# Optimization experiments

Measured on AMD Instinct MI355X. Metric: run time of the kernel, lower is better.

## Reference

```python
import jax, jax.numpy as jnp
import numpy as np
import math

B, N, DIM = 2, 4096, 256
NUM_HEADS = 8
HEAD_DIM = DIM // NUM_HEADS
WINDOW = 7  # default window_size in create_local_mask


def local_mask(seq_len: int, window_size: int = WINDOW) -> jnp.ndarray:
    """Boolean [N,N] mask: True where attention is allowed (2D grid locality)."""
    grid = int(math.isqrt(seq_len))
    idx = jnp.arange(seq_len)
    row, col = idx // grid, idx % grid
    half = window_size // 2
    ok_row = jnp.abs(row[:, None] - row[None, :]) <= half
    ok_col = jnp.abs(col[:, None] - col[None, :]) <= half
    return ok_row & ok_col


def setup_inputs() -> dict:
    key = jax.random.key(0)
    k1, k2, k3, k4 = jax.random.split(key, 4)
    x = jax.random.normal(k1, (B, N, DIM), dtype=jnp.float32)
    W_qkv = jax.random.normal(k2, (3 * DIM, DIM), dtype=jnp.float32) * (DIM ** -0.5)
    W_proj = jax.random.normal(k3, (DIM, DIM), dtype=jnp.float32) * (DIM ** -0.5)
    b_proj = jax.random.normal(k4, (DIM,), dtype=jnp.float32) * 0.01
    temperature = jnp.ones((1,), dtype=jnp.float32)
    return {"x": x, "W_qkv": W_qkv, "W_proj": W_proj, "b_proj": b_proj,
            "temperature": temperature}


def reference(x, W_qkv, W_proj, b_proj, temperature):
    Bb, Nn, C = x.shape
    scale = HEAD_DIM ** -0.5
    # qkv linear (no bias): [B,N,3C] -> [3,B,H,N,hd]
    qkv = (x @ W_qkv.T).reshape(Bb, Nn, 3, NUM_HEADS, HEAD_DIM)
    qkv = jnp.transpose(qkv, (2, 0, 3, 1, 4))
    q, k, v = qkv[0], qkv[1], qkv[2]
    # scores with learnable temperature
    attn = jnp.einsum('bhqd,bhkd->bhqk', q, k) * (scale * temperature[0])
    mask = local_mask(Nn)  # training path: N > 100 -> mask applied
    attn = jnp.where(mask[None, None, :, :], attn, -jnp.inf)
    attn = jax.nn.softmax(attn, axis=-1)
    out = jnp.einsum('bhqk,bhkd->bhqd', attn, v)  # [B,H,N,hd]
    out = jnp.transpose(out, (0, 2, 1, 3)).reshape(Bb, Nn, C)
    return out @ W_proj.T + b_proj
```

## Files before the change

kernel.cpp:

```cpp
#include <hip/hip_runtime.h>
#include <hip/hip_bf16.h>
#include <hip/hip_fp16.h>
#include <math.h>

#define DIM   256
#define NHEAD 8
#define HD    32
#define NTOK  4096
#define GRD   64
#define BATCH 2
#define MTOT  (BATCH * NTOK)

typedef __attribute__((ext_vector_type(8))) short bf16x8;
typedef __attribute__((ext_vector_type(4))) float f32x4;
typedef _Float16 h8 __attribute__((ext_vector_type(8)));
typedef _Float16 h2v __attribute__((ext_vector_type(2)));

#if defined(__has_builtin)
#if __has_builtin(__builtin_amdgcn_fdot2)
#define HAVE_DOT2 1
#endif
#endif
#ifndef HAVE_DOT2
#define HAVE_DOT2 0
#endif

static __device__ __forceinline__ unsigned short f2b(float f) {
  __hip_bfloat16 h = __float2bfloat16(f);
  union { __hip_bfloat16 h; unsigned short u; } cv;
  cv.h = h;
  return cv.u;
}

static __device__ __forceinline__ bf16x8 pack8(float4 a0, float4 a1) {
  union { bf16x8 v; unsigned short u[8]; } o;
  o.u[0] = f2b(a0.x); o.u[1] = f2b(a0.y); o.u[2] = f2b(a0.z); o.u[3] = f2b(a0.w);
  o.u[4] = f2b(a1.x); o.u[5] = f2b(a1.y); o.u[6] = f2b(a1.z); o.u[7] = f2b(a1.w);
  return o.v;
}

__global__ __launch_bounds__(256) void gemm_qkv(const float* __restrict__ A,
                                                const float* __restrict__ Bw,
                                                _Float16* __restrict__ Cout) {
  const int K = 256, N = 768;
  __shared__ __hip_bfloat16 As[128 * 40];
  __shared__ __hip_bfloat16 Bs[128 * 40];
  const int tid = threadIdx.x;
  const int l = tid & 63, w = tid >> 6;
  const int bm = blockIdx.y * 128, bn = blockIdx.x * 128;
  const int wr = w >> 1, wc = w & 1;
  const int lr = l & 15, kh = l >> 4;
  const int lrow = l >> 2, lcol = (l & 3) * 8;

  f32x4 acc[4][4];
  #pragma unroll
  for (int i = 0; i < 4; ++i)
    #pragma unroll
    for (int j = 0; j < 4; ++j)
      acc[i][j] = (f32x4){0.f, 0.f, 0.f, 0.f};

  for (int k0 = 0; k0 < K; k0 += 32) {
    #pragma unroll
    for (int i = 0; i < 2; ++i) {
      const int r0 = (w * 2 + i) * 16;
      const float* ga = A  + (size_t)(bm + r0 + lrow) * K + k0 + lcol;
      const float* gb = Bw + (size_t)(bn + r0 + lrow) * K + k0 + lcol;
      float4 a0 = *(const float4*)ga, a1 = *(const float4*)(ga + 4);
      float4 b0 = *(const float4*)gb, b1 = *(const float4*)(gb + 4);
      *(bf16x8*)&As[(r0 + lrow) * 40 + lcol] = pack8(a0, a1);
      *(bf16x8*)&Bs[(r0 + lrow) * 40 + lcol] = pack8(b0, b1);
    }
    __syncthreads();

    bf16x8 af[4], bfr[4];
    #pragma unroll
    for (int f = 0; f < 4; ++f) {
      af[f]  = *(const bf16x8*)&As[(wr * 64 + f * 16 + lr) * 40 + kh * 8];
      bfr[f] = *(const bf16x8*)&Bs[(wc * 64 + f * 16 + lr) * 40 + kh * 8];
    }
    #pragma unroll
    for (int fi = 0; fi < 4; ++fi)
      #pragma unroll
      for (int fj = 0; fj < 4; ++fj)
        acc[fi][fj] = __builtin_amdgcn_mfma_f32_16x16x32_bf16(af[fi], bfr[fj], acc[fi][fj], 0, 0, 0);
    __syncthreads();
  }

  #pragma unroll
  for (int fi = 0; fi < 4; ++fi)
    #pragma unroll
    for (int fj = 0; fj < 4; ++fj)
      #pragma unroll
      for (int rr = 0; rr < 4; ++rr) {
        const int m = bm + wr * 64 + fi * 16 + kh * 4 + rr;
        const int n = bn + wc * 64 + fj * 16 + lr;
        const int sel = n >> 8, rem = n & 255;
        const int hh = rem >> 5, d = rem & 31;
        const int bb = m >> 12, tok = m & 4095;
        Cout[((size_t)(sel * 16 + bb * 8 + hh) * NTOK + tok) * HD + d] =
            (_Float16)acc[fi][fj][rr];
      }
}

__global__ __launch_bounds__(256) void gemm_proj(const __hip_bfloat16* __restrict__ A,
                                                 const float* __restrict__ Bw,
                                                 const float* __restrict__ bias,
                                                 float* __restrict__ Cout) {
  const int K = 256, N = 256;
  __shared__ __hip_bfloat16 As[128 * 32];
  __shared__ __hip_bfloat16 Bs[128 * 40];
  const int tid = threadIdx.x;
  const int l = tid & 63, w = tid >> 6;
  const int bm = blockIdx.y * 128, bn = blockIdx.x * 128;
  const int wr = w >> 1, wc = w & 1;
  const int lr = l & 15, kh = l >> 4;
  const int lrow = l >> 2, lcol = (l & 3) * 8;

  f32x4 acc[4][4];
  #pragma unroll
  for (int i = 0; i < 4; ++i)
    #pragma unroll
    for (int j = 0; j < 4; ++j)
      acc[i][j] = (f32x4){0.f, 0.f, 0.f, 0.f};

  for (int k0 = 0; k0 < K; k0 += 32) {
    #pragma unroll
    for (int i = 0; i < 2; ++i) {
      const int r0 = (w * 2 + i) * 16;
      const __hip_bfloat16* ga = A + (size_t)(bm + r0 + lrow) * K + k0 + lcol;
      __builtin_amdgcn_global_load_lds(
          (const __attribute__((address_space(1))) void*)ga,
          (__attribute__((address_space(3))) void*)&As[r0 * 32], 16, 0, 0);
      const float* gb = Bw + (size_t)(bn + r0 + lrow) * K + k0 + lcol;
      float4 b0 = *(const float4*)gb, b1 = *(const float4*)(gb + 4);
      *(bf16x8*)&Bs[(r0 + lrow) * 40 + lcol] = pack8(b0, b1);
    }
    __syncthreads();

    bf16x8 af[4], bfr[4];
    #pragma unroll
    for (int f = 0; f < 4; ++f) {
      af[f]  = *(const bf16x8*)&As[(wr * 64 + f * 16 + lr) * 32 + kh * 8];
      bfr[f] = *(const bf16x8*)&Bs[(wc * 64 + f * 16 + lr) * 40 + kh * 8];
    }
    #pragma unroll
    for (int fi = 0; fi < 4; ++fi)
      #pragma unroll
      for (int fj = 0; fj < 4; ++fj)
        acc[fi][fj] = __builtin_amdgcn_mfma_f32_16x16x32_bf16(af[fi], bfr[fj], acc[fi][fj], 0, 0, 0);
    __syncthreads();
  }

  #pragma unroll
  for (int fi = 0; fi < 4; ++fi)
    #pragma unroll
    for (int fj = 0; fj < 4; ++fj)
      #pragma unroll
      for (int rr = 0; rr < 4; ++rr) {
        const int m = bm + wr * 64 + fi * 16 + kh * 4 + rr;
        const int n = bn + wc * 64 + fj * 16 + lr;
        Cout[(size_t)m * N + n] = acc[fi][fj][rr] + bias[n];
      }
}

__global__ __launch_bounds__(512) void local_attn(const _Float16* __restrict__ qkv,
                                                  const float* __restrict__ temp,
                                                  __hip_bfloat16* __restrict__ attn_out) {
  __shared__ _Float16 Ks[512 * 32];
  __shared__ _Float16 Vs[512 * 32];

  const int P = blockIdx.x;
  const int L = (P & 7) * 64 + (P >> 3);
  const int plane = L >> 5, rp = L & 31;
  const int b = plane >> 3, h = plane & 7;
  const int t = threadIdx.x;
  const int qr = t >> 8, c = (t >> 2) & 63, s = t & 3;
  const int r = rp * 2 + qr;

  const float scale = 0.17677669529663687f * temp[0];

  const _Float16* qplane = qkv + (size_t)(b * 8 + h) * (NTOK * HD);
  const _Float16* kplane = qkv + (size_t)(16 + b * 8 + h) * (NTOK * HD);
  const _Float16* vplane = qkv + (size_t)(32 + b * 8 + h) * (NTOK * HD);

  {
    const int rbase = rp * 2 - 3;
    const int wbase = t & ~63;
    #pragma unroll
    for (int i = 0; i < 4; ++i) {
      const int id = i * 512 + t;
      const int drp = id >> 8;
      const int tokloc = (id >> 2) & 63;
      const int jjp = id & 3;
      const int x = ((tokloc >> 1) ^ drp) & 3;
      const int jj = jjp ^ x;
      int row = rbase + drp;
      row = row < 0 ? 0 : (row > 63 ? 63 : row);
      const _Float16* src = kplane + (size_t)row * 2048 + tokloc * 32 + jj * 8;
      const _Float16* srv = vplane + (size_t)row * 2048 + tokloc * 32 + jj * 8;
      const int dbase = (i * 512 + wbase) * 8;
      __builtin_amdgcn_global_load_lds(
          (const __attribute__((address_space(1))) void*)src,
          (__attribute__((address_space(3))) void*)&Ks[dbase], 16, 0, 0);
      __builtin_amdgcn_global_load_lds(
          (const __attribute__((address_space(1))) void*)srv,
          (__attribute__((address_space(3))) void*)&Vs[dbase], 16, 0, 0);
    }
  }

  union { h8 v; h2v p[4]; } qu[4];
  {
    const _Float16* qrp_ = qplane + (size_t)(r * GRD + c) * HD;
    #pragma unroll
    for (int jj = 0; jj < 4; ++jj) qu[jj].v = *(const h8*)&qrp_[jj * 8];
  }
  __syncthreads();

  const char* KB = (const char*)Ks;
  const char* VB = (const char*)Vs;
  float sc[14];
  int bs[14];
  float mx = -INFINITY;
  const int ndr = (s < 3) ? 2 : 1;
  #pragma unroll
  for (int i = 0; i < 2; ++i) {
    const int dr = s - 3 + 4 * i;
    const int drp = dr + 3 + qr;
    const int rr = r + dr;
    const bool rowok = (i < ndr) && (rr >= 0) && (rr < GRD);
    #pragma unroll
    for (int dc = -3; dc <= 3; ++dc) {
      const int cc = c + dc;
      const bool ok = rowok && (cc >= 0) && (cc < GRD);
      int tk = drp * 64 + cc;
      tk = tk < 0 ? 0 : (tk > 511 ? 511 : tk);
      const int x = ((tk >> 1) ^ (tk >> 6)) & 3;
      const int sb = (tk << 6) ^ (x << 4);
      bs[i * 7 + dc + 3] = sb;
      float dot = 0.f;
      #pragma unroll
      for (int jj = 0; jj < 4; ++jj) {
        union { h8 v; h2v p[4]; } kk;
        kk.v = *(const h8*)(KB + (sb ^ (jj << 4)));
        #pragma unroll
        for (int kx = 0; kx < 4; ++kx) {
#if HAVE_DOT2
          dot = __builtin_amdgcn_fdot2(kk.p[kx], qu[jj].p[kx], dot, false);
#else
          dot = fmaf((float)kk.p[kx][0], (float)qu[jj].p[kx][0], dot);
          dot = fmaf((float)kk.p[kx][1], (float)qu[jj].p[kx][1], dot);
#endif
        }
      }
      const float v = ok ? dot * scale : -INFINITY;
      sc[i * 7 + dc + 3] = v;
      mx = fmaxf(mx, v);
    }
  }

  mx = fmaxf(mx, __shfl_xor(mx, 1));
  mx = fmaxf(mx, __shfl_xor(mx, 2));

  float psum = 0.f;
  #pragma unroll
  for (int i = 0; i < 14; ++i) {
    float e = __expf(sc[i] - mx);
    sc[i] = e;
    psum += e;
  }
  psum += __shfl_xor(psum, 1);
  psum += __shfl_xor(psum, 2);
  const float inv = 1.0f / psum;

  float o[HD];
  #pragma unroll
  for (int i = 0; i < HD; ++i) o[i] = 0.f;

  #pragma unroll
  for (int e = 0; e < 14; ++e) {
    const float p = sc[e];
    const int sb = bs[e];
    #pragma unroll
    for (int jj = 0; jj < 4; ++jj) {
      union { h8 v; h2v p2[4]; } vv;
      vv.v = *(const h8*)(VB + (sb ^ (jj << 4)));
      #pragma unroll
      for (int kx = 0; kx < 4; ++kx) {
        o[jj * 8 + kx * 2 + 0] = fmaf(p, (float)vv.p2[kx][0], o[jj * 8 + kx * 2 + 0]);
        o[jj * 8 + kx * 2 + 1] = fmaf(p, (float)vv.p2[kx][1], o[jj * 8 + kx * 2 + 1]);
      }
    }
  }

  #pragma unroll
  for (int d = 0; d < HD; ++d) {
    o[d] += __shfl_xor(o[d], 1);
    o[d] += __shfl_xor(o[d], 2);
  }

  union { uint4 u; unsigned short sh[8]; } pk;
  #pragma unroll
  for (int j = 0; j < 8; ++j) pk.sh[j] = f2b(o[s * 8 + j] * inv);
  __hip_bfloat16* dst = attn_out + ((size_t)(b * NTOK + r * GRD + c)) * DIM + h * HD + s * 8;
  *(uint4*)dst = pk.u;
}

extern "C" void kernel_launch(void* const* d_in, const int* in_sizes, int n_in,
                              void* d_out, int out_size, void* d_ws, size_t ws_size,
                              hipStream_t stream) {
  const float* x     = (const float*)d_in[0];
  const float* Wqkv  = (const float*)d_in[1];
  const float* Wproj = (const float*)d_in[2];
  const float* bproj = (const float*)d_in[3];
  const float* temp  = (const float*)d_in[4];
  float* out = (float*)d_out;

  char* ws = (char*)d_ws;
  _Float16* qkv_f16       = (_Float16*)ws;
  __hip_bfloat16* attn_bf = (__hip_bfloat16*)(ws + 25165824);

  {
    dim3 grid(3 * DIM / 128, MTOT / 128);
    gemm_qkv<<<grid, 256, 0, stream>>>(x, Wqkv, qkv_f16);
  }
  local_attn<<<BATCH * NHEAD * (GRD / 2), 512, 0, stream>>>(qkv_f16, temp, attn_bf);

  {
    dim3 grid(DIM / 128, MTOT / 128);
    gemm_proj<<<grid, 256, 0, stream>>>(attn_bf, Wproj, bproj, out);
  }
}
```

Measured before the change: 49.79 us.

## Shrink GEMM M-tiles to 64 and redistribute attention PV work across lanes

```diff
diff --git a/kernel.cpp b/kernel.cpp
--- a/kernel.cpp
+++ b/kernel.cpp
@@ -15,6 +15,7 @@
 typedef __attribute__((ext_vector_type(4))) float f32x4;
 typedef _Float16 h8 __attribute__((ext_vector_type(8)));
 typedef _Float16 h2v __attribute__((ext_vector_type(2)));
+typedef __fp16 fp16x2 __attribute__((ext_vector_type(2)));
 
 #if defined(__has_builtin)
 #if __has_builtin(__builtin_amdgcn_fdot2)
@@ -42,44 +43,47 @@
 __global__ __launch_bounds__(256) void gemm_qkv(const float* __restrict__ A,
                                                 const float* __restrict__ Bw,
                                                 _Float16* __restrict__ Cout) {
-  const int K = 256, N = 768;
-  __shared__ __hip_bfloat16 As[128 * 40];
+  const int K = 256;
+  __shared__ __hip_bfloat16 As[64 * 40];
   __shared__ __hip_bfloat16 Bs[128 * 40];
   const int tid = threadIdx.x;
   const int l = tid & 63, w = tid >> 6;
-  const int bm = blockIdx.y * 128, bn = blockIdx.x * 128;
+  const int bm = blockIdx.y * 64, bn = blockIdx.x * 128;
   const int wr = w >> 1, wc = w & 1;
   const int lr = l & 15, kh = l >> 4;
-  const int lrow = l >> 2, lcol = (l & 3) * 8;
-
-  f32x4 acc[4][4];
-  #pragma unroll
-  for (int i = 0; i < 4; ++i)
+  const int lrow = tid >> 2, lcol = (tid & 3) * 8;
+
+  f32x4 acc[2][4];
+  #pragma unroll
+  for (int i = 0; i < 2; ++i)
     #pragma unroll
     for (int j = 0; j < 4; ++j)
       acc[i][j] = (f32x4){0.f, 0.f, 0.f, 0.f};
 
   for (int k0 = 0; k0 < K; k0 += 32) {
+    {
+      const float* ga = A + (size_t)(bm + lrow) * K + k0 + lcol;
+      float4 a0 = *(const float4*)ga, a1 = *(const float4*)(ga + 4);
+      *(bf16x8*)&As[lrow * 40 + lcol] = pack8(a0, a1);
+    }
     #pragma unroll
     for (int i = 0; i < 2; ++i) {
-      const int r0 = (w * 2 + i) * 16;
-      const float* ga = A  + (size_t)(bm + r0 + lrow) * K + k0 + lcol;
-      const float* gb = Bw + (size_t)(bn + r0 + lrow) * K + k0 + lcol;
-      float4 a0 = *(const float4*)ga, a1 = *(const float4*)(ga + 4);
+      const int row = i * 64 + lrow;
+      const float* gb = Bw + (size_t)(bn + row) * K + k0 + lcol;
       float4 b0 = *(const float4*)gb, b1 = *(const float4*)(gb + 4);
-      *(bf16x8*)&As[(r0 + lrow) * 40 + lcol] = pack8(a0, a1);
-      *(bf16x8*)&Bs[(r0 + lrow) * 40 + lcol] = pack8(b0, b1);
+      *(bf16x8*)&Bs[row * 40 + lcol] = pack8(b0, b1);
     }
     __syncthreads();
 
-    bf16x8 af[4], bfr[4];
-    #pragma unroll
-    for (int f = 0; f < 4; ++f) {
-      af[f]  = *(const bf16x8*)&As[(wr * 64 + f * 16 + lr) * 40 + kh * 8];
+    bf16x8 af[2], bfr[4];
+    #pragma unroll
+    for (int f = 0; f < 2; ++f)
+      af[f] = *(const bf16x8*)&As[(wr * 32 + f * 16 + lr) * 40 + kh * 8];
+    #pragma unroll
+    for (int f = 0; f < 4; ++f)
       bfr[f] = *(const bf16x8*)&Bs[(wc * 64 + f * 16 + lr) * 40 + kh * 8];
-    }
-    #pragma unroll
-    for (int fi = 0; fi < 4; ++fi)
+    #pragma unroll
+    for (int fi = 0; fi < 2; ++fi)
       #pragma unroll
       for (int fj = 0; fj < 4; ++fj)
         acc[fi][fj] = __builtin_amdgcn_mfma_f32_16x16x32_bf16(af[fi], bfr[fj], acc[fi][fj], 0, 0, 0);
@@ -87,12 +91,12 @@
   }
 
   #pragma unroll
-  for (int fi = 0; fi < 4; ++fi)
+  for (int fi = 0; fi < 2; ++fi)
     #pragma unroll
     for (int fj = 0; fj < 4; ++fj)
       #pragma unroll
       for (int rr = 0; rr < 4; ++rr) {
-        const int m = bm + wr * 64 + fi * 16 + kh * 4 + rr;
+        const int m = bm + wr * 32 + fi * 16 + kh * 4 + rr;
         const int n = bn + wc * 64 + fj * 16 + lr;
         const int sel = n >> 8, rem = n & 255;
         const int hh = rem >> 5, d = rem & 31;
@@ -107,44 +111,47 @@
                                                  const float* __restrict__ bias,
                                                  float* __restrict__ Cout) {
   const int K = 256, N = 256;
-  __shared__ __hip_bfloat16 As[128 * 32];
+  __shared__ __hip_bfloat16 As[64 * 32];
   __shared__ __hip_bfloat16 Bs[128 * 40];
   const int tid = threadIdx.x;
   const int l = tid & 63, w = tid >> 6;
-  const int bm = blockIdx.y * 128, bn = blockIdx.x * 128;
+  const int bm = blockIdx.y * 64, bn = blockIdx.x * 128;
   const int wr = w >> 1, wc = w & 1;
   const int lr = l & 15, kh = l >> 4;
-  const int lrow = l >> 2, lcol = (l & 3) * 8;
-
-  f32x4 acc[4][4];
-  #pragma unroll
-  for (int i = 0; i < 4; ++i)
+  const int lrow = tid >> 2, lcol = (tid & 3) * 8;
+
+  f32x4 acc[2][4];
+  #pragma unroll
+  for (int i = 0; i < 2; ++i)
     #pragma unroll
     for (int j = 0; j < 4; ++j)
       acc[i][j] = (f32x4){0.f, 0.f, 0.f, 0.f};
 
   for (int k0 = 0; k0 < K; k0 += 32) {
-    #pragma unroll
-    for (int i = 0; i < 2; ++i) {
-      const int r0 = (w * 2 + i) * 16;
-      const __hip_bfloat16* ga = A + (size_t)(bm + r0 + lrow) * K + k0 + lcol;
+    {
+      const __hip_bfloat16* ga = A + (size_t)(bm + lrow) * K + k0 + lcol;
       __builtin_amdgcn_global_load_lds(
           (const __attribute__((address_space(1))) void*)ga,
-          (__attribute__((address_space(3))) void*)&As[r0 * 32], 16, 0, 0);
-      const float* gb = Bw + (size_t)(bn + r0 + lrow) * K + k0 + lcol;
+          (__attribute__((address_space(3))) void*)&As[w * 512], 16, 0, 0);
+    }
+    #pragma unroll
+    for (int i = 0; i < 2; ++i) {
+      const int row = i * 64 + lrow;
+      const float* gb = Bw + (size_t)(bn + row) * K + k0 + lcol;
       float4 b0 = *(const float4*)gb, b1 = *(const float4*)(gb + 4);
-      *(bf16x8*)&Bs[(r0 + lrow) * 40 + lcol] = pack8(b0, b1);
+      *(bf16x8*)&Bs[row * 40 + lcol] = pack8(b0, b1);
     }
     __syncthreads();
 
-    bf16x8 af[4], bfr[4];
-    #pragma unroll
-    for (int f = 0; f < 4; ++f) {
-      af[f]  = *(const bf16x8*)&As[(wr * 64 + f * 16 + lr) * 32 + kh * 8];
+    bf16x8 af[2], bfr[4];
+    #pragma unroll
+    for (int f = 0; f < 2; ++f)
+      af[f] = *(const bf16x8*)&As[(wr * 32 + f * 16 + lr) * 32 + kh * 8];
+    #pragma unroll
+    for (int f = 0; f < 4; ++f)
       bfr[f] = *(const bf16x8*)&Bs[(wc * 64 + f * 16 + lr) * 40 + kh * 8];
-    }
-    #pragma unroll
-    for (int fi = 0; fi < 4; ++fi)
+    #pragma unroll
+    for (int fi = 0; fi < 2; ++fi)
       #pragma unroll
       for (int fj = 0; fj < 4; ++fj)
         acc[fi][fj] = __builtin_amdgcn_mfma_f32_16x16x32_bf16(af[fi], bfr[fj], acc[fi][fj], 0, 0, 0);
@@ -152,12 +159,12 @@
   }
 
   #pragma unroll
-  for (int fi = 0; fi < 4; ++fi)
+  for (int fi = 0; fi < 2; ++fi)
     #pragma unroll
     for (int fj = 0; fj < 4; ++fj)
       #pragma unroll
       for (int rr = 0; rr < 4; ++rr) {
-        const int m = bm + wr * 64 + fi * 16 + kh * 4 + rr;
+        const int m = bm + wr * 32 + fi * 16 + kh * 4 + rr;
         const int n = bn + wc * 64 + fj * 16 + lr;
         Cout[(size_t)m * N + n] = acc[fi][fj][rr] + bias[n];
       }
@@ -219,7 +226,6 @@
   const char* KB = (const char*)Ks;
   const char* VB = (const char*)Vs;
   float sc[14];
-  int bs[14];
   float mx = -INFINITY;
   const int ndr = (s < 3) ? 2 : 1;
   #pragma unroll
@@ -236,7 +242,6 @@
       tk = tk < 0 ? 0 : (tk > 511 ? 511 : tk);
       const int x = ((tk >> 1) ^ (tk >> 6)) & 3;
       const int sb = (tk << 6) ^ (x << 4);
-      bs[i * 7 + dc + 3] = sb;
       float dot = 0.f;
       #pragma unroll
       for (int jj = 0; jj < 4; ++jj) {
@@ -272,35 +277,55 @@
   psum += __shfl_xor(psum, 2);
   const float inv = 1.0f / psum;
 
-  float o[HD];
-  #pragma unroll
-  for (int i = 0; i < HD; ++i) o[i] = 0.f;
-
-  #pragma unroll
-  for (int e = 0; e < 14; ++e) {
-    const float p = sc[e];
-    const int sb = bs[e];
-    #pragma unroll
-    for (int jj = 0; jj < 4; ++jj) {
-      union { h8 v; h2v p2[4]; } vv;
-      vv.v = *(const h8*)(VB + (sb ^ (jj << 4)));
-      #pragma unroll
-      for (int kx = 0; kx < 4; ++kx) {
-        o[jj * 8 + kx * 2 + 0] = fmaf(p, (float)vv.p2[kx][0], o[jj * 8 + kx * 2 + 0]);
-        o[jj * 8 + kx * 2 + 1] = fmaf(p, (float)vv.p2[kx][1], o[jj * 8 + kx * 2 + 1]);
+  unsigned int mine[7], r1v[7], r2a[7], r2b[7];
+  #pragma unroll
+  for (int j = 0; j < 7; ++j) {
+    fp16x2 hp = __builtin_amdgcn_cvt_pkrtz(sc[2 * j] * inv, sc[2 * j + 1] * inv);
+    union { fp16x2 h; unsigned int u; } cv; cv.h = hp;
+    mine[j] = cv.u;
+  }
+  #pragma unroll
+  for (int j = 0; j < 7; ++j) r1v[j] = (unsigned)__shfl_xor((int)mine[j], 1);
+  #pragma unroll
+  for (int j = 0; j < 7; ++j) r2a[j] = (unsigned)__shfl_xor((int)mine[j], 2);
+  #pragma unroll
+  for (int j = 0; j < 7; ++j) r2b[j] = (unsigned)__shfl_xor((int)r1v[j], 2);
+
+  float o[8];
+  #pragma unroll
+  for (int i = 0; i < 8; ++i) o[i] = 0.f;
+
+  #pragma unroll
+  for (int ss = 0; ss < 4; ++ss) {
+    const unsigned int* set = (ss == 0) ? mine : (ss == 1) ? r1v
+                             : (ss == 2) ? r2a : r2b;
+    const int sp = s ^ ss;
+    #pragma unroll
+    for (int j = 0; j < 7; ++j) {
+      union { unsigned int u; h2v h; } pp; pp.u = set[j];
+      #pragma unroll
+      for (int half = 0; half < 2; ++half) {
+        const int slot = 2 * j + half;
+        const int ii = slot / 7;
+        const int dc = (slot % 7) - 3;
+        const float p = (float)pp.h[half];
+        int tk = (sp + 4 * ii + qr) * 64 + c + dc;
+        tk = tk < 0 ? 0 : (tk > 511 ? 511 : tk);
+        const int x = ((tk >> 1) ^ (tk >> 6)) & 3;
+        union { h8 v; h2v p2[4]; } vv;
+        vv.v = *(const h8*)(VB + (tk << 6) + (((s ^ x) & 3) << 4));
+        #pragma unroll
+        for (int kx = 0; kx < 4; ++kx) {
+          o[kx * 2 + 0] = fmaf(p, (float)vv.p2[kx][0], o[kx * 2 + 0]);
+          o[kx * 2 + 1] = fmaf(p, (float)vv.p2[kx][1], o[kx * 2 + 1]);
+        }
       }
     }
   }
 
-  #pragma unroll
-  for (int d = 0; d < HD; ++d) {
-    o[d] += __shfl_xor(o[d], 1);
-    o[d] += __shfl_xor(o[d], 2);
-  }
-
   union { uint4 u; unsigned short sh[8]; } pk;
   #pragma unroll
-  for (int j = 0; j < 8; ++j) pk.sh[j] = f2b(o[s * 8 + j] * inv);
+  for (int j = 0; j < 8; ++j) pk.sh[j] = f2b(o[j]);
   __hip_bfloat16* dst = attn_out + ((size_t)(b * NTOK + r * GRD + c)) * DIM + h * HD + s * 8;
   *(uint4*)dst = pk.u;
 }
@@ -320,13 +345,13 @@
   __hip_bfloat16* attn_bf = (__hip_bfloat16*)(ws + 25165824);
 
   {
-    dim3 grid(3 * DIM / 128, MTOT / 128);
+    dim3 grid(3 * DIM / 128, MTOT / 64);
     gemm_qkv<<<grid, 256, 0, stream>>>(x, Wqkv, qkv_f16);
   }
   local_attn<<<BATCH * NHEAD * (GRD / 2), 512, 0, stream>>>(qkv_f16, temp, attn_bf);
 
   {
-    dim3 grid(DIM / 128, MTOT / 128);
+    dim3 grid(DIM / 128, MTOT / 64);
     gemm_proj<<<grid, 256, 0, stream>>>(attn_bf, Wproj, bproj, out);
   }
 }
```

Measured after the change: 110.1 us. +121.2%, slower.

## Rewrite local attention with bf16 MFMA and online softmax, transposed V layout

Applied to the files above, without the earlier changes.

```diff
diff --git a/kernel.cpp b/kernel.cpp
--- a/kernel.cpp
+++ b/kernel.cpp
@@ -1,6 +1,5 @@
 #include <hip/hip_runtime.h>
 #include <hip/hip_bf16.h>
-#include <hip/hip_fp16.h>
 #include <math.h>
 
 #define DIM   256
@@ -10,20 +9,10 @@
 #define GRD   64
 #define BATCH 2
 #define MTOT  (BATCH * NTOK)
+#define PLANE (NTOK * HD)
 
 typedef __attribute__((ext_vector_type(8))) short bf16x8;
 typedef __attribute__((ext_vector_type(4))) float f32x4;
-typedef _Float16 h8 __attribute__((ext_vector_type(8)));
-typedef _Float16 h2v __attribute__((ext_vector_type(2)));
-
-#if defined(__has_builtin)
-#if __has_builtin(__builtin_amdgcn_fdot2)
-#define HAVE_DOT2 1
-#endif
-#endif
-#ifndef HAVE_DOT2
-#define HAVE_DOT2 0
-#endif
 
 static __device__ __forceinline__ unsigned short f2b(float f) {
   __hip_bfloat16 h = __float2bfloat16(f);
@@ -32,6 +21,12 @@
   return cv.u;
 }
 
+static __device__ __forceinline__ unsigned cvtpk_bf16(float lo, float hi) {
+  unsigned r;
+  asm("v_cvt_pk_bf16_f32 %0, %1, %2" : "=v"(r) : "v"(lo), "v"(hi));
+  return r;
+}
+
 static __device__ __forceinline__ bf16x8 pack8(float4 a0, float4 a1) {
   union { bf16x8 v; unsigned short u[8]; } o;
   o.u[0] = f2b(a0.x); o.u[1] = f2b(a0.y); o.u[2] = f2b(a0.z); o.u[3] = f2b(a0.w);
@@ -39,12 +34,17 @@
   return o.v;
 }
 
+#define GLDS16(SRC, DST) __builtin_amdgcn_global_load_lds( \
+    (const __attribute__((address_space(1))) void*)(SRC),  \
+    (__attribute__((address_space(3))) void*)(DST), 16, 0, 0)
+
 __global__ __launch_bounds__(256) void gemm_qkv(const float* __restrict__ A,
                                                 const float* __restrict__ Bw,
-                                                _Float16* __restrict__ Cout) {
-  const int K = 256, N = 768;
-  __shared__ __hip_bfloat16 As[128 * 40];
-  __shared__ __hip_bfloat16 Bs[128 * 40];
+                                                unsigned short* __restrict__ Cout) {
+  const int K = 256;
+  __shared__ __align__(16) char smem[34816];
+  __hip_bfloat16* As = (__hip_bfloat16*)smem;
+  __hip_bfloat16* Bs = (__hip_bfloat16*)(smem + 10240);
   const int tid = threadIdx.x;
   const int l = tid & 63, w = tid >> 6;
   const int bm = blockIdx.y * 128, bn = blockIdx.x * 128;
@@ -86,20 +86,48 @@
     __syncthreads();
   }
 
-  #pragma unroll
-  for (int fi = 0; fi < 4; ++fi)
-    #pragma unroll
-    for (int fj = 0; fj < 4; ++fj)
-      #pragma unroll
-      for (int rr = 0; rr < 4; ++rr) {
-        const int m = bm + wr * 64 + fi * 16 + kh * 4 + rr;
-        const int n = bn + wc * 64 + fj * 16 + lr;
-        const int sel = n >> 8, rem = n & 255;
-        const int hh = rem >> 5, d = rem & 31;
-        const int bb = m >> 12, tok = m & 4095;
-        Cout[((size_t)(sel * 16 + bb * 8 + hh) * NTOK + tok) * HD + d] =
-            (_Float16)acc[fi][fj][rr];
-      }
+  if (blockIdx.x < 4) {
+    #pragma unroll
+    for (int fi = 0; fi < 4; ++fi)
+      #pragma unroll
+      for (int fj = 0; fj < 4; ++fj)
+        #pragma unroll
+        for (int rr = 0; rr < 4; ++rr) {
+          const int m = bm + wr * 64 + fi * 16 + kh * 4 + rr;
+          const int n = bn + wc * 64 + fj * 16 + lr;
+          const int sel = n >> 8, rem = n & 255;
+          const int hh = rem >> 5, d = rem & 31;
+          const int bb = m >> 12, tok = m & 4095;
+          Cout[(size_t)(sel * 16 + bb * 8 + hh) * PLANE + tok * 32 + d] =
+              f2b(acc[fi][fj][rr]);
+        }
+  } else {
+    unsigned short* Ts = (unsigned short*)smem;
+    #pragma unroll
+    for (int fi = 0; fi < 4; ++fi)
+      #pragma unroll
+      for (int fj = 0; fj < 4; ++fj)
+        #pragma unroll
+        for (int rr = 0; rr < 4; ++rr) {
+          const int tokl = wr * 64 + fi * 16 + kh * 4 + rr;
+          const int dl   = wc * 64 + fj * 16 + lr;
+          Ts[tokl * 136 + dl] = f2b(acc[fi][fj][rr]);
+        }
+    __syncthreads();
+    const int dl = tid >> 1, th = (tid & 1) * 64;
+    const int dg = (bn - 512) + dl;
+    const int hh = dg >> 5, dd = dg & 31;
+    const int bb = bm >> 12, tokb = bm & 4095;
+    unsigned short* vt = Cout + (size_t)(32 + bb * 8 + hh) * PLANE + dd * 4096 + tokb + th;
+    #pragma unroll
+    for (int j = 0; j < 8; ++j) {
+      union { bf16x8 v; unsigned short u[8]; } o;
+      #pragma unroll
+      for (int e = 0; e < 8; ++e)
+        o.u[e] = Ts[(th + j * 8 + e) * 136 + dl];
+      *(bf16x8*)(vt + j * 8) = o.v;
+    }
+  }
 }
 
 __global__ __launch_bounds__(256) void gemm_proj(const __hip_bfloat16* __restrict__ A,
@@ -128,9 +156,7 @@
     for (int i = 0; i < 2; ++i) {
       const int r0 = (w * 2 + i) * 16;
       const __hip_bfloat16* ga = A + (size_t)(bm + r0 + lrow) * K + k0 + lcol;
-      __builtin_amdgcn_global_load_lds(
-          (const __attribute__((address_space(1))) void*)ga,
-          (__attribute__((address_space(3))) void*)&As[r0 * 32], 16, 0, 0);
+      GLDS16(ga, &As[r0 * 32]);
       const float* gb = Bw + (size_t)(bn + r0 + lrow) * K + k0 + lcol;
       float4 b0 = *(const float4*)gb, b1 = *(const float4*)(gb + 4);
       *(bf16x8*)&Bs[(r0 + lrow) * 40 + lcol] = pack8(b0, b1);
@@ -163,146 +189,145 @@
       }
 }
 
-__global__ __launch_bounds__(512) void local_attn(const _Float16* __restrict__ qkv,
-                                                  const float* __restrict__ temp,
-                                                  __hip_bfloat16* __restrict__ attn_out) {
-  __shared__ _Float16 Ks[512 * 32];
-  __shared__ _Float16 Vs[512 * 32];
+__global__ __launch_bounds__(256) void local_attn_mfma(
+    const unsigned short* __restrict__ qkv, const float* __restrict__ temp,
+    unsigned short* __restrict__ attn_out) {
+  __shared__ __align__(16) unsigned short Ks[448 * 32];
+  __shared__ __align__(16) unsigned short Vt[32 * 512];
 
   const int P = blockIdx.x;
-  const int L = (P & 7) * 64 + (P >> 3);
-  const int plane = L >> 5, rp = L & 31;
-  const int b = plane >> 3, h = plane & 7;
-  const int t = threadIdx.x;
-  const int qr = t >> 8, c = (t >> 2) & 63, s = t & 3;
-  const int r = rp * 2 + qr;
+  const int L = (P & 7) * 128 + (P >> 3);
+  const int b = L >> 9, h = (L >> 6) & 7, r = L & 63;
+  const int tid = threadIdx.x;
+  const int l = tid & 63, wv = tid >> 6;
+  const int q15 = l & 15, sg = l >> 4;
 
   const float scale = 0.17677669529663687f * temp[0];
 
-  const _Float16* qplane = qkv + (size_t)(b * 8 + h) * (NTOK * HD);
-  const _Float16* kplane = qkv + (size_t)(16 + b * 8 + h) * (NTOK * HD);
-  const _Float16* vplane = qkv + (size_t)(32 + b * 8 + h) * (NTOK * HD);
-
-  {
-    const int rbase = rp * 2 - 3;
-    const int wbase = t & ~63;
-    #pragma unroll
-    for (int i = 0; i < 4; ++i) {
-      const int id = i * 512 + t;
-      const int drp = id >> 8;
-      const int tokloc = (id >> 2) & 63;
-      const int jjp = id & 3;
-      const int x = ((tokloc >> 1) ^ drp) & 3;
-      const int jj = jjp ^ x;
-      int row = rbase + drp;
-      row = row < 0 ? 0 : (row > 63 ? 63 : row);
-      const _Float16* src = kplane + (size_t)row * 2048 + tokloc * 32 + jj * 8;
-      const _Float16* srv = vplane + (size_t)row * 2048 + tokloc * 32 + jj * 8;
-      const int dbase = (i * 512 + wbase) * 8;
-      __builtin_amdgcn_global_load_lds(
-          (const __attribute__((address_space(1))) void*)src,
-          (__attribute__((address_space(3))) void*)&Ks[dbase], 16, 0, 0);
-      __builtin_amdgcn_global_load_lds(
-          (const __attribute__((address_space(1))) void*)srv,
-          (__attribute__((address_space(3))) void*)&Vs[dbase], 16, 0, 0);
-    }
-  }
-
-  union { h8 v; h2v p[4]; } qu[4];
-  {
-    const _Float16* qrp_ = qplane + (size_t)(r * GRD + c) * HD;
-    #pragma unroll
-    for (int jj = 0; jj < 4; ++jj) qu[jj].v = *(const h8*)&qrp_[jj * 8];
-  }
+  const unsigned short* qplane  = qkv + (size_t)(b * 8 + h) * PLANE;
+  const unsigned short* kplane  = qplane + (size_t)16 * PLANE;
+  const unsigned short* vtplane = qplane + (size_t)32 * PLANE;
+
+  #pragma unroll
+  for (int i = 0; i < 7; ++i) {
+    const int ch = i * 256 + tid;
+    const int tok = ch >> 2, jjp = ch & 3;
+    const int ri = tok >> 6, kloc = tok & 63;
+    int rr = r - 3 + ri; rr = rr < 0 ? 0 : (rr > 63 ? 63 : rr);
+    const int jl = jjp ^ ((tok >> 1) & 3);
+    const unsigned short* src = kplane + (size_t)(rr * 64 + kloc) * 32 + jl * 8;
+    GLDS16(src, &Ks[(i * 256 + (tid & ~63)) * 8]);
+  }
+  #pragma unroll
+  for (int i = 0; i < 8; ++i) {
+    const int ch = i * 256 + tid;
+    const int d = ch >> 6, chp = ch & 63;
+    const int chl = chp ^ (d & 7);
+    const int ri = chl >> 3, part = chl & 7;
+    int rr = r - 3 + ri; rr = rr < 0 ? 0 : (rr > 63 ? 63 : rr);
+    const unsigned short* src = vtplane + (size_t)d * 4096 + rr * 64 + part * 8;
+    GLDS16(src, &Vt[(i * 256 + (tid & ~63)) * 8]);
+  }
+
+  const bf16x8 qf = *(const bf16x8*)(qplane + (size_t)(r * 64 + wv * 16 + q15) * 32 + sg * 8);
+
   __syncthreads();
 
-  const char* KB = (const char*)Ks;
-  const char* VB = (const char*)Vs;
-  float sc[14];
-  int bs[14];
-  float mx = -INFINITY;
-  const int ndr = (s < 3) ? 2 : 1;
-  #pragma unroll
-  for (int i = 0; i < 2; ++i) {
-    const int dr = s - 3 + 4 * i;
-    const int drp = dr + 3 + qr;
-    const int rr = r + dr;
-    const bool rowok = (i < ndr) && (rr >= 0) && (rr < GRD);
-    #pragma unroll
-    for (int dc = -3; dc <= 3; ++dc) {
-      const int cc = c + dc;
-      const bool ok = rowok && (cc >= 0) && (cc < GRD);
-      int tk = drp * 64 + cc;
-      tk = tk < 0 ? 0 : (tk > 511 ? 511 : tk);
-      const int x = ((tk >> 1) ^ (tk >> 6)) & 3;
-      const int sb = (tk << 6) ^ (x << 4);
-      bs[i * 7 + dc + 3] = sb;
-      float dot = 0.f;
-      #pragma unroll
-      for (int jj = 0; jj < 4; ++jj) {
-        union { h8 v; h2v p[4]; } kk;
-        kk.v = *(const h8*)(KB + (sb ^ (jj << 4)));
-        #pragma unroll
-        for (int kx = 0; kx < 4; ++kx) {
-#if HAVE_DOT2
-          dot = __builtin_amdgcn_fdot2(kk.p[kx], qu[jj].p[kx], dot, false);
-#else
-          dot = fmaf((float)kk.p[kx][0], (float)qu[jj].p[kx][0], dot);
-          dot = fmaf((float)kk.p[kx][1], (float)qu[jj].p[kx][1], dot);
-#endif
-        }
+  const int qcol = wv * 16 + q15;
+  float m_run = -INFINITY, l_run = 0.f;
+  f32x4 Od[2];
+  Od[0] = (f32x4){0.f, 0.f, 0.f, 0.f};
+  Od[1] = (f32x4){0.f, 0.f, 0.f, 0.f};
+  const f32x4 zf = {0.f, 0.f, 0.f, 0.f};
+  const int laA = ((l >> 4) & 1) * 32 + q15;
+  const int laB = laA + 16;
+  const bool hiG = (l & 32) != 0;
+
+  #pragma unroll
+  for (int c = 0; c < 7; ++c) {
+    const int rr_c = r - 3 + c;
+    if (rr_c >= 0 && rr_c <= 63) {
+      f32x4 st[4];
+      #pragma unroll
+      for (int kt = 0; kt < 4; ++kt) {
+        const int tok = c * 64 + kt * 16 + q15;
+        const bf16x8 kf = *(const bf16x8*)((const char*)Ks + tok * 64 +
+                                           ((sg ^ ((tok >> 1) & 3)) << 4));
+        st[kt] = __builtin_amdgcn_mfma_f32_16x16x32_bf16(kf, qf, zf, 0, 0, 0);
       }
-      const float v = ok ? dot * scale : -INFINITY;
-      sc[i * 7 + dc + 3] = v;
-      mx = fmaxf(mx, v);
-    }
-  }
-
-  mx = fmaxf(mx, __shfl_xor(mx, 1));
-  mx = fmaxf(mx, __shfl_xor(mx, 2));
-
-  float psum = 0.f;
-  #pragma unroll
-  for (int i = 0; i < 14; ++i) {
-    float e = __expf(sc[i] - mx);
-    sc[i] = e;
-    psum += e;
-  }
-  psum += __shfl_xor(psum, 1);
-  psum += __shfl_xor(psum, 2);
-  const float inv = 1.0f / psum;
-
-  float o[HD];
-  #pragma unroll
-  for (int i = 0; i < HD; ++i) o[i] = 0.f;
-
-  #pragma unroll
-  for (int e = 0; e < 14; ++e) {
-    const float p = sc[e];
-    const int sb = bs[e];
-    #pragma unroll
-    for (int jj = 0; jj < 4; ++jj) {
-      union { h8 v; h2v p2[4]; } vv;
-      vv.v = *(const h8*)(VB + (sb ^ (jj << 4)));
-      #pragma unroll
-      for (int kx = 0; kx < 4; ++kx) {
-        o[jj * 8 + kx * 2 + 0] = fmaf(p, (float)vv.p2[kx][0], o[jj * 8 + kx * 2 + 0]);
-        o[jj * 8 + kx * 2 + 1] = fmaf(p, (float)vv.p2[kx][1], o[jj * 8 + kx * 2 + 1]);
+      float mc = -INFINITY;
+      #pragma unroll
+      for (int kt = 0; kt < 4; ++kt)
+        #pragma unroll
+        for (int rg = 0; rg < 4; ++rg) {
+          const int keyloc = kt * 16 + sg * 4 + rg;
+          const bool ok = (unsigned)(keyloc - qcol + 3) <= 6u;
+          const float v = ok ? st[kt][rg] * scale : -INFINITY;
+          st[kt][rg] = v;
+          mc = fmaxf(mc, v);
+        }
+      mc = fmaxf(mc, __shfl_xor(mc, 16));
+      mc = fmaxf(mc, __shfl_xor(mc, 32));
+      const float mnew = fmaxf(m_run, mc);
+      const float alpha = __expf(m_run - mnew);
+      float lc = 0.f;
+      #pragma unroll
+      for (int kt = 0; kt < 4; ++kt)
+        #pragma unroll
+        for (int rg = 0; rg < 4; ++rg) {
+          const float e = __expf(st[kt][rg] - mnew);
+          st[kt][rg] = e;
+          lc += e;
+        }
+      lc += __shfl_xor(lc, 16);
+      lc += __shfl_xor(lc, 32);
+      l_run = l_run * alpha + lc;
+      m_run = mnew;
+      Od[0] *= alpha;
+      Od[1] *= alpha;
+
+      unsigned pkw[8];
+      #pragma unroll
+      for (int kt = 0; kt < 4; ++kt) {
+        pkw[kt * 2 + 0] = cvtpk_bf16(st[kt][0], st[kt][1]);
+        pkw[kt * 2 + 1] = cvtpk_bf16(st[kt][2], st[kt][3]);
       }
-    }
-  }
-
-  #pragma unroll
-  for (int d = 0; d < HD; ++d) {
-    o[d] += __shfl_xor(o[d], 1);
-    o[d] += __shfl_xor(o[d], 2);
-  }
-
-  union { uint4 u; unsigned short sh[8]; } pk;
-  #pragma unroll
-  for (int j = 0; j < 8; ++j) pk.sh[j] = f2b(o[s * 8 + j] * inv);
-  __hip_bfloat16* dst = attn_out + ((size_t)(b * NTOK + r * GRD + c)) * DIM + h * HD + s * 8;
-  *(uint4*)dst = pk.u;
+      #pragma unroll
+      for (int hf = 0; hf < 2; ++hf) {
+        unsigned wA[2], wB[2];
+        #pragma unroll
+        for (int w2 = 0; w2 < 2; ++w2) {
+          const unsigned a0 = (unsigned)__shfl((int)pkw[(2 * hf) * 2 + w2], laA);
+          const unsigned a1 = (unsigned)__shfl((int)pkw[(2 * hf + 1) * 2 + w2], laA);
+          wA[w2] = hiG ? a1 : a0;
+          const unsigned b0 = (unsigned)__shfl((int)pkw[(2 * hf) * 2 + w2], laB);
+          const unsigned b1 = (unsigned)__shfl((int)pkw[(2 * hf + 1) * 2 + w2], laB);
+          wB[w2] = hiG ? b1 : b0;
+        }
+        union { unsigned u[4]; bf16x8 v; } pf;
+        pf.u[0] = wA[0]; pf.u[1] = wA[1]; pf.u[2] = wB[0]; pf.u[3] = wB[1];
+        #pragma unroll
+        for (int dt = 0; dt < 2; ++dt) {
+          const int d = dt * 16 + q15;
+          const int chl = c * 8 + hf * 4 + sg;
+          const bf16x8 vf = *(const bf16x8*)((const char*)Vt + d * 1024 +
+                                             ((chl ^ (d & 7)) << 4));
+          Od[dt] = __builtin_amdgcn_mfma_f32_16x16x32_bf16(vf, pf.v, Od[dt], 0, 0, 0);
+        }
+      }
+    }
+  }
+
+  const float invl = 1.0f / l_run;
+  #pragma unroll
+  for (int dt = 0; dt < 2; ++dt) {
+    const unsigned w0 = cvtpk_bf16(Od[dt][0] * invl, Od[dt][1] * invl);
+    const unsigned w1 = cvtpk_bf16(Od[dt][2] * invl, Od[dt][3] * invl);
+    unsigned short* dst = attn_out + (size_t)(b * 4096 + r * 64 + qcol) * 256 +
+                          h * 32 + dt * 16 + sg * 4;
+    uint2 uu; uu.x = w0; uu.y = w1;
+    *(uint2*)dst = uu;
+  }
 }
 
 extern "C" void kernel_launch(void* const* d_in, const int* in_sizes, int n_in,
@@ -316,15 +341,15 @@
   float* out = (float*)d_out;
 
   char* ws = (char*)d_ws;
-  _Float16* qkv_f16       = (_Float16*)ws;
+  unsigned short* qkv_bf  = (unsigned short*)ws;
   __hip_bfloat16* attn_bf = (__hip_bfloat16*)(ws + 25165824);
 
   {
     dim3 grid(3 * DIM / 128, MTOT / 128);
-    gemm_qkv<<<grid, 256, 0, stream>>>(x, Wqkv, qkv_f16);
-  }
-  local_attn<<<BATCH * NHEAD * (GRD / 2), 512, 0, stream>>>(qkv_f16, temp, attn_bf);
-
+    gemm_qkv<<<grid, 256, 0, stream>>>(x, Wqkv, qkv_bf);
+  }
+  local_attn_mfma<<<BATCH * NHEAD * GRD, 256, 0, stream>>>(qkv_bf, temp,
+                                                           (unsigned short*)attn_bf);
   {
     dim3 grid(DIM / 128, MTOT / 128);
     gemm_proj<<<grid, 256, 0, stream>>>(attn_bf, Wproj, bproj, out);
```

Result: no change. 50.64 us (+1.7%).
